# Performance work log

Hardware: AMD Instinct MI355X
Metric: run time of the kernel (lower is better)

## Reference

```python
import jax, jax.numpy as jnp
import numpy as np

EPS = 1e-7  # K.epsilon()
ROUTINGS = 3

def squash(v):
    # v: [..., dim_capsule]
    s2 = jnp.sum(jnp.square(v), axis=-1, keepdims=True)
    scale = s2 / (1.0 + s2) / jnp.sqrt(s2 + EPS)
    return scale * v

def setup_inputs() -> dict:
    key = jax.random.key(0)
    k1, k2 = jax.random.split(key)
    B, IN_CAPS, IN_DIM = 256, 1152, 8
    NUM_CAPS, DIM_CAPS = 10, 16
    inputs = jax.random.normal(k1, (B, IN_CAPS, IN_DIM), dtype=jnp.float32)
    W = jax.random.normal(k2, (NUM_CAPS, IN_CAPS, DIM_CAPS, IN_DIM), dtype=jnp.float32) * 0.05
    return {"inputs": inputs, "W": W}

def reference(inputs, W):
    # inputs: [B, I, Q]; W: [J, I, P, Q]
    # inputs_hat[b,j,i,p] = sum_q W[j,i,p,q] * inputs[b,i,q]
    inputs_hat = jnp.einsum('jipq,biq->bjip', W, inputs)  # [B, J, I, P]
    B, J, I, P = inputs_hat.shape
    b = jnp.zeros((B, J, I), dtype=inputs_hat.dtype)
    outputs = None
    for r in range(ROUTINGS):
        c = jax.nn.softmax(b, axis=1)                      # over num_capsule J
        s = jnp.einsum('bji,bjip->bjp', c, inputs_hat)     # [B, J, P]
        outputs = squash(s)
        if r < ROUTINGS - 1:
            b = b + jnp.einsum('bjp,bjip->bji', outputs, inputs_hat)
    return outputs
```

## Files before the change

kernel.cpp:

```cpp
#include <hip/hip_runtime.h>

typedef _Float16 h2 __attribute__((ext_vector_type(2)));
typedef _Float16 h8 __attribute__((ext_vector_type(8)));
typedef float f4 __attribute__((ext_vector_type(4)));

#define BB 256
#define II 1152
#define QQ 8
#define JJ 10
#define PP 16

#define BT 16
#define IT 8
#define NBT (BB / BT)
#define NIT (II / IT)
#define XRH 72
#define WTILE (IT * PP * QQ)

#define NW (JJ * II * PP * QQ)
#define NX (BB * II * QQ)
#define NS (BB * JJ * PP)
#define LOG2E 1.4426950408889634f

template <int CTRL>
__device__ __forceinline__ float dpp_add(float v) {
    int s = __builtin_bit_cast(int, v);
    int t = __builtin_amdgcn_update_dpp(0, s, CTRL, 0xF, 0xF, true);
    return v + __builtin_bit_cast(float, t);
}
__device__ __forceinline__ float row_sum16(float v) {
    v = dpp_add<0xB1>(v);
    v = dpp_add<0x4E>(v);
    v = dpp_add<0x124>(v);
    v = dpp_add<0x128>(v);
    return v;
}

__device__ __forceinline__ float dot8(h8 w, h8 x) {
    h2 w0 = __builtin_shufflevector(w, w, 0, 1), w1 = __builtin_shufflevector(w, w, 2, 3);
    h2 w2 = __builtin_shufflevector(w, w, 4, 5), w3 = __builtin_shufflevector(w, w, 6, 7);
    h2 x0 = __builtin_shufflevector(x, x, 0, 1), x1 = __builtin_shufflevector(x, x, 2, 3);
    h2 x2 = __builtin_shufflevector(x, x, 4, 5), x3 = __builtin_shufflevector(x, x, 6, 7);
    float acc = __builtin_amdgcn_fdot2(w0, x0, 0.0f, false);
    acc = __builtin_amdgcn_fdot2(w1, x1, acc, false);
    acc = __builtin_amdgcn_fdot2(w2, x2, acc, false);
    acc = __builtin_amdgcn_fdot2(w3, x3, acc, false);
    return acc;
}

__global__ __launch_bounds__(256) void prep_kernel(
    const float* __restrict__ X, const float* __restrict__ W,
    _Float16* __restrict__ Xh, _Float16* __restrict__ Wh,
    float* __restrict__ S)
{
    const int g = blockIdx.x * 256 + threadIdx.x;
    const int stride = gridDim.x * 256;
    typedef _Float16 h4 __attribute__((ext_vector_type(4)));
    for (int k = g; k < NW / 4; k += stride) {
        const float4 f = ((const float4*)W)[k];
        h4 o = { (_Float16)f.x, (_Float16)f.y, (_Float16)f.z, (_Float16)f.w };
        ((h4*)Wh)[k] = o;
    }
    for (int k = g; k < NX / 4; k += stride) {
        const float4 f = ((const float4*)X)[k];
        h4 o = { (_Float16)f.x, (_Float16)f.y, (_Float16)f.z, (_Float16)f.w };
        ((h4*)Xh)[k] = o;
    }
    const float4 z = {0.f, 0.f, 0.f, 0.f};
    for (int k = g; k < 3 * NS / 4; k += stride) ((float4*)S)[k] = z;
}

__global__ __launch_bounds__(256) void s0_mfma_kernel(
    const _Float16* __restrict__ Xh, const _Float16* __restrict__ Wh,
    float* __restrict__ S0)
{
    const int wid  = blockIdx.x * 4 + (threadIdx.x >> 6);
    const int lane = threadIdx.x & 63;
    const int bt  = wid / 80;
    const int rem = wid % 80;
    const int j   = rem >> 3;
    const int kc  = rem & 7;
    const int b0  = bt * 16;
    const int m    = lane & 15;
    const int quad = lane >> 4;
    const int ib   = kc * 144;

    const _Float16* ax = Xh + ((size_t)(b0 + m) * II + ib + quad) * QQ;
    const _Float16* bw = Wh + (((size_t)j * II + ib + quad) * PP + m) * QQ;

    f4 acc = {0.f, 0.f, 0.f, 0.f};
    for (int t = 0; t < 36; ++t) {
        const h8 a = *(const h8*)ax;
        const h8 b = *(const h8*)bw;
        acc = __builtin_amdgcn_mfma_f32_16x16x32_f16(a, b, acc, 0, 0, 0);
        ax += 4 * QQ;
        bw += (size_t)4 * PP * QQ;
    }
#pragma unroll
    for (int r = 0; r < 4; ++r) {
        const int row = quad * 4 + r;
        atomicAdd(&S0[((size_t)(b0 + row) * JJ + j) * PP + m], 0.1f * acc[r]);
    }
}

template <int R>
__global__ __launch_bounds__(256, 4) void pass_kernel(
    const _Float16* __restrict__ Xh,
    const _Float16* __restrict__ Wh,
    const float* __restrict__ Sprev,
    float* __restrict__ V0,
    float* __restrict__ Sout)
{
    __shared__ _Float16 ws[JJ * WTILE];
    __shared__ _Float16 xs[BT * XRH];

    const int bt = blockIdx.x & (NBT - 1);
    const int it = blockIdx.x >> 4;
    const int b0 = bt * BT;
    const int i0 = it * IT;
    const int tid = threadIdx.x;

    {
        const size_t jstride = (size_t)II * PP * QQ;
        const _Float16* wsrc = Wh + (size_t)i0 * PP * QQ;
#pragma unroll
        for (int k = 0; k < 5; ++k) {
            const int c = tid + k * 256;
            const int j = c >> 7;
            const int r = c & 127;
            *(h8*)(ws + j * WTILE + r * 8) = *(const h8*)(wsrc + j * jstride + r * 8);
        }
        if (tid < 128) {
            const int xb = tid >> 3;
            const int xr = tid & 7;
            *(h8*)(xs + xb * XRH + xr * 8) =
                *(const h8*)(Xh + ((size_t)(b0 + xb) * II + i0) * QQ + xr * 8);
        }
    }
    __syncthreads();

    const int b_l = tid >> 4;
    const int p   = tid & 15;
    const int b   = b0 + b_l;

    float vv[JJ];
#pragma unroll
    for (int j = 0; j < JJ; ++j) {
        const float sp = Sprev[((size_t)b * JJ + j) * PP + p];
        const float n2 = row_sum16(sp * sp);
        const float scale = n2 * __builtin_amdgcn_rcpf(1.0f + n2)
                               * __builtin_amdgcn_rsqf(n2 + 1e-7f);
        float v = sp * scale;
        if (R == 1) {
            if (it == 0) V0[((size_t)b * JJ + j) * PP + p] = v;
        } else {
            v += V0[((size_t)b * JJ + j) * PP + p];
        }
        vv[j] = v * LOG2E;
    }

    float sacc[JJ];
#pragma unroll
    for (int j = 0; j < JJ; ++j) sacc[j] = 0.0f;

    const _Float16* wb = ws + p * QQ;
    const _Float16* xb = xs + b_l * XRH;

#pragma unroll
    for (int i = 0; i < IT; ++i) {
        const h8 x8 = *(const h8*)(xb + i * QQ);

        float h[JJ];
#pragma unroll
        for (int j = 0; j < JJ; ++j)
            h[j] = dot8(*(const h8*)(wb + j * WTILE + i * PP * QQ), x8);

        float e[JJ];
#pragma unroll
        for (int j = 0; j < JJ; ++j) {
            const float bj = row_sum16(vv[j] * h[j]);
            e[j] = __builtin_amdgcn_exp2f(bj);
        }
        float s01 = e[0] + e[1], s23 = e[2] + e[3], s45 = e[4] + e[5],
              s67 = e[6] + e[7], s89 = e[8] + e[9];
        float t0 = s01 + s23, t1 = s45 + s67;
        const float sum = (t0 + t1) + s89;
        const float inv = __builtin_amdgcn_rcpf(sum);
#pragma unroll
        for (int j = 0; j < JJ; ++j) sacc[j] += (e[j] * inv) * h[j];
    }

#pragma unroll
    for (int j = 0; j < JJ; ++j)
        atomicAdd(&Sout[((size_t)b * JJ + j) * PP + p], sacc[j]);
}

__global__ __launch_bounds__(256) void squash_out_kernel(const float* __restrict__ S,
                                                         float* __restrict__ V)
{
    const int idx = blockIdx.x * blockDim.x + threadIdx.x;
    if (idx >= BB * JJ) return;
    const float4* sp = (const float4*)(S + idx * PP);
    float4 a = sp[0], b4 = sp[1], c4 = sp[2], d4 = sp[3];
    float s2 = a.x * a.x + a.y * a.y + a.z * a.z + a.w * a.w +
               b4.x * b4.x + b4.y * b4.y + b4.z * b4.z + b4.w * b4.w +
               c4.x * c4.x + c4.y * c4.y + c4.z * c4.z + c4.w * c4.w +
               d4.x * d4.x + d4.y * d4.y + d4.z * d4.z + d4.w * d4.w;
    const float scale = s2 / (1.0f + s2) / sqrtf(s2 + 1e-7f);
    a.x *= scale; a.y *= scale; a.z *= scale; a.w *= scale;
    b4.x *= scale; b4.y *= scale; b4.z *= scale; b4.w *= scale;
    c4.x *= scale; c4.y *= scale; c4.z *= scale; c4.w *= scale;
    d4.x *= scale; d4.y *= scale; d4.z *= scale; d4.w *= scale;
    float4* vp = (float4*)(V + idx * PP);
    vp[0] = a; vp[1] = b4; vp[2] = c4; vp[3] = d4;
}

extern "C" void kernel_launch(void* const* d_in, const int* in_sizes, int n_in,
                              void* d_out, int out_size, void* d_ws, size_t ws_size,
                              hipStream_t stream)
{
    const float* X = (const float*)d_in[0];
    const float* W = (const float*)d_in[1];
    float* out = (float*)d_out;

    _Float16* Xh = (_Float16*)d_ws;
    _Float16* Wh = Xh + NX;
    float* S0 = (float*)(Wh + NW);
    float* S1 = S0 + NS;
    float* S2 = S1 + NS;
    float* v0 = S2 + NS;

    const int grid = NBT * NIT;

    prep_kernel<<<1024, 256, 0, stream>>>(X, W, Xh, Wh, S0);
    s0_mfma_kernel<<<320, 256, 0, stream>>>(Xh, Wh, S0);
    pass_kernel<1><<<grid, 256, 0, stream>>>(Xh, Wh, S0, v0, S1);
    pass_kernel<2><<<grid, 256, 0, stream>>>(Xh, Wh, S1, v0, S2);
    squash_out_kernel<<<10, 256, 0, stream>>>(S2, out);
}
```

Measured before the change: 134.2 us.

## Move routing pass dot products onto MFMA using transposed fp16 weight copy

Rewrites the routing pass kernel so both the agreement logits (v·W·x) and the weighted sum into S use 16x16x32 f16 MFMA instructions instead of per-thread fdot2 loops with DPP row reductions. To feed the first MFMA, the prep kernel now also writes a transposed fp16 copy of W (p innermost). The block no longer stages W in shared memory but reads W directly from global, and it keeps x transposed in fp32 in LDS. The transpose uses uncoalesced scalar reads of W in prep. The pass also issues more atomics and rounds the routing coefficients and v to fp16, which may cost precision.

```diff
diff --git a/kernel.cpp b/kernel.cpp
--- a/kernel.cpp
+++ b/kernel.cpp
@@ -15,11 +15,14 @@
 #define NBT (BB / BT)
 #define NIT (II / IT)
 #define XRH 72
-#define WTILE (IT * PP * QQ)
+#define VHR 168
+#define XTQ 17
+#define XTI 136
 
 #define NW (JJ * II * PP * QQ)
 #define NX (BB * II * QQ)
 #define NS (BB * JJ * PP)
+#define JSTRIDE ((size_t)II * PP * QQ)
 #define LOG2E 1.4426950408889634f
 
 template <int CTRL>
@@ -35,23 +38,15 @@
     v = dpp_add<0x128>(v);
     return v;
 }
-
-__device__ __forceinline__ float dot8(h8 w, h8 x) {
-    h2 w0 = __builtin_shufflevector(w, w, 0, 1), w1 = __builtin_shufflevector(w, w, 2, 3);
-    h2 w2 = __builtin_shufflevector(w, w, 4, 5), w3 = __builtin_shufflevector(w, w, 6, 7);
-    h2 x0 = __builtin_shufflevector(x, x, 0, 1), x1 = __builtin_shufflevector(x, x, 2, 3);
-    h2 x2 = __builtin_shufflevector(x, x, 4, 5), x3 = __builtin_shufflevector(x, x, 6, 7);
-    float acc = __builtin_amdgcn_fdot2(w0, x0, 0.0f, false);
-    acc = __builtin_amdgcn_fdot2(w1, x1, acc, false);
-    acc = __builtin_amdgcn_fdot2(w2, x2, acc, false);
-    acc = __builtin_amdgcn_fdot2(w3, x3, acc, false);
-    return acc;
+__device__ __forceinline__ float swz_xor16(float v) {
+    int s = __builtin_bit_cast(int, v);
+    return __builtin_bit_cast(float, __builtin_amdgcn_ds_swizzle(s, 0x401F));
 }
 
 __global__ __launch_bounds__(256) void prep_kernel(
     const float* __restrict__ X, const float* __restrict__ W,
     _Float16* __restrict__ Xh, _Float16* __restrict__ Wh,
-    float* __restrict__ S)
+    _Float16* __restrict__ Wt, float* __restrict__ S)
 {
     const int g = blockIdx.x * 256 + threadIdx.x;
     const int stride = gridDim.x * 256;
@@ -60,6 +55,10 @@
         const float4 f = ((const float4*)W)[k];
         h4 o = { (_Float16)f.x, (_Float16)f.y, (_Float16)f.z, (_Float16)f.w };
         ((h4*)Wh)[k] = o;
+    }
+    for (int k = g; k < NW; k += stride) {
+        const int p = k & 15, q = (k >> 4) & 7, ji = k >> 7;
+        Wt[k] = (_Float16)W[((size_t)ji * 16 + p) * 8 + q];
     }
     for (int k = g; k < NX / 4; k += stride) {
         const float4 f = ((const float4*)X)[k];
@@ -97,22 +96,22 @@
         bw += (size_t)4 * PP * QQ;
     }
 #pragma unroll
-    for (int r = 0; r < 4; ++r) {
-        const int row = quad * 4 + r;
-        atomicAdd(&S0[((size_t)(b0 + row) * JJ + j) * PP + m], 0.1f * acc[r]);
-    }
+    for (int r = 0; r < 4; ++r)
+        atomicAdd(&S0[((size_t)(b0 + quad * 4 + r) * JJ + j) * PP + m], 0.1f * acc[r]);
 }
 
 template <int R>
 __global__ __launch_bounds__(256, 4) void pass_kernel(
     const _Float16* __restrict__ Xh,
     const _Float16* __restrict__ Wh,
+    const _Float16* __restrict__ Wt,
     const float* __restrict__ Sprev,
     float* __restrict__ V0,
     float* __restrict__ Sout)
 {
-    __shared__ _Float16 ws[JJ * WTILE];
     __shared__ _Float16 xs[BT * XRH];
+    __shared__ float    xT[IT * XTI];
+    __shared__ _Float16 vh[BT * VHR];
 
     const int bt = blockIdx.x & (NBT - 1);
     const int it = blockIdx.x >> 4;
@@ -120,79 +119,92 @@
     const int i0 = it * IT;
     const int tid = threadIdx.x;
 
+    if (tid < 128) {
+        const int xb = tid >> 3, xr = tid & 7;
+        *(h8*)(xs + xb * XRH + xr * 8) =
+            *(const h8*)(Xh + ((size_t)(b0 + xb) * II + i0) * QQ + xr * 8);
+    }
+#pragma unroll
+    for (int r = 0; r < 4; ++r) {
+        const int idx = tid + r * 256;
+        const int b = idx & 15, q = (idx >> 4) & 7, il = idx >> 7;
+        xT[il * XTI + q * XTQ + b] =
+            (float)Xh[((size_t)(b0 + b) * II + i0 + il) * QQ + q];
+    }
     {
-        const size_t jstride = (size_t)II * PP * QQ;
-        const _Float16* wsrc = Wh + (size_t)i0 * PP * QQ;
-#pragma unroll
-        for (int k = 0; k < 5; ++k) {
-            const int c = tid + k * 256;
-            const int j = c >> 7;
-            const int r = c & 127;
-            *(h8*)(ws + j * WTILE + r * 8) = *(const h8*)(wsrc + j * jstride + r * 8);
+        const int b_l = tid >> 4, p = tid & 15;
+        const int b = b0 + b_l;
+#pragma unroll
+        for (int j = 0; j < JJ; ++j) {
+            const float sp = Sprev[((size_t)b * JJ + j) * PP + p];
+            const float n2 = row_sum16(sp * sp);
+            const float sc = n2 * __builtin_amdgcn_rcpf(1.0f + n2)
+                                * __builtin_amdgcn_rsqf(n2 + 1e-7f);
+            float v = sp * sc;
+            if (R == 1) {
+                if (it == 0) V0[((size_t)b * JJ + j) * PP + p] = v;
+            } else {
+                v += V0[((size_t)b * JJ + j) * PP + p];
+            }
+            vh[b_l * VHR + j * 16 + p] = (_Float16)(v * LOG2E);
         }
-        if (tid < 128) {
-            const int xb = tid >> 3;
-            const int xr = tid & 7;
-            *(h8*)(xs + xb * XRH + xr * 8) =
-                *(const h8*)(Xh + ((size_t)(b0 + xb) * II + i0) * QQ + xr * 8);
-        }
     }
     __syncthreads();
 
-    const int b_l = tid >> 4;
-    const int p   = tid & 15;
-    const int b   = b0 + b_l;
-
-    float vv[JJ];
+    const int lane = tid & 63;
+    const int wv   = tid >> 6;
+    const int quad = lane >> 4;
+    const int l15  = lane & 15;
+    const h8 hz = {(_Float16)0, (_Float16)0, (_Float16)0, (_Float16)0,
+                   (_Float16)0, (_Float16)0, (_Float16)0, (_Float16)0};
+
+    const int il = 2 * wv + (quad >> 1);
+    float xv0, xv1, xv2, xv3;
+    {
+        const float* xp = xT + il * XTI + ((quad & 1) * 4) * XTQ + l15;
+        xv0 = xp[0]; xv1 = xp[XTQ]; xv2 = xp[2 * XTQ]; xv3 = xp[3 * XTQ];
+    }
+    const int iA = i0 + 2 * wv + (l15 >> 3);
+    const _Float16* abase = Wt + ((size_t)iA * QQ + (l15 & 7)) * PP + (quad & 1) * 8;
+    const _Float16* vbase = vh + l15 * VHR + (quad & 1) * 8;
+
+    float lg[JJ];
 #pragma unroll
     for (int j = 0; j < JJ; ++j) {
-        const float sp = Sprev[((size_t)b * JJ + j) * PP + p];
-        const float n2 = row_sum16(sp * sp);
-        const float scale = n2 * __builtin_amdgcn_rcpf(1.0f + n2)
-                               * __builtin_amdgcn_rsqf(n2 + 1e-7f);
-        float v = sp * scale;
-        if (R == 1) {
-            if (it == 0) V0[((size_t)b * JJ + j) * PP + p] = v;
-        } else {
-            v += V0[((size_t)b * JJ + j) * PP + p];
-        }
-        vv[j] = v * LOG2E;
-    }
-
-    float sacc[JJ];
-#pragma unroll
-    for (int j = 0; j < JJ; ++j) sacc[j] = 0.0f;
-
-    const _Float16* wb = ws + p * QQ;
-    const _Float16* xb = xs + b_l * XRH;
-
-#pragma unroll
-    for (int i = 0; i < IT; ++i) {
-        const h8 x8 = *(const h8*)(xb + i * QQ);
-
-        float h[JJ];
-#pragma unroll
-        for (int j = 0; j < JJ; ++j)
-            h[j] = dot8(*(const h8*)(wb + j * WTILE + i * PP * QQ), x8);
-
-        float e[JJ];
-#pragma unroll
-        for (int j = 0; j < JJ; ++j) {
-            const float bj = row_sum16(vv[j] * h[j]);
-            e[j] = __builtin_amdgcn_exp2f(bj);
-        }
-        float s01 = e[0] + e[1], s23 = e[2] + e[3], s45 = e[4] + e[5],
-              s67 = e[6] + e[7], s89 = e[8] + e[9];
-        float t0 = s01 + s23, t1 = s45 + s67;
-        const float sum = (t0 + t1) + s89;
-        const float inv = __builtin_amdgcn_rcpf(sum);
-#pragma unroll
-        for (int j = 0; j < JJ; ++j) sacc[j] += (e[j] * inv) * h[j];
-    }
-
-#pragma unroll
-    for (int j = 0; j < JJ; ++j)
-        atomicAdd(&Sout[((size_t)b * JJ + j) * PP + p], sacc[j]);
+        const h8 a  = *(const h8*)(abase + (size_t)j * JSTRIDE);
+        h8 bv = *(const h8*)(vbase + j * 16);
+        if (quad >= 2) bv = hz;
+        f4 acc = {0.f, 0.f, 0.f, 0.f};
+        acc = __builtin_amdgcn_mfma_f32_16x16x32_f16(a, bv, acc, 0, 0, 0);
+        const float part = acc[0] * xv0 + acc[1] * xv1 + acc[2] * xv2 + acc[3] * xv3;
+        lg[j] = part + swz_xor16(part);
+    }
+
+    float e[JJ];
+#pragma unroll
+    for (int j = 0; j < JJ; ++j) e[j] = __builtin_amdgcn_exp2f(lg[j]);
+    float s01 = e[0] + e[1], s23 = e[2] + e[3], s45 = e[4] + e[5],
+          s67 = e[6] + e[7], s89 = e[8] + e[9];
+    const float sum = ((s01 + s23) + (s45 + s67)) + s89;
+    const float inv = __builtin_amdgcn_rcpf(sum);
+
+    const int ig = i0 + 2 * wv + (quad >> 1);
+    const h8 x8 = *(const h8*)(xs + l15 * XRH + (2 * wv + (quad >> 1)) * 8);
+    const _Float16* bbase = Wh + ((size_t)ig * PP + l15) * QQ;
+
+#pragma unroll
+    for (int j = 0; j < JJ; ++j) {
+        const _Float16 ch = (_Float16)(e[j] * inv);
+        const h8 cs8 = {ch, ch, ch, ch, ch, ch, ch, ch};
+        const h8 a2 = x8 * cs8;
+        h8 b2 = *(const h8*)(bbase + (size_t)j * JSTRIDE);
+        if (quad & 1) b2 = hz;
+        f4 acc = {0.f, 0.f, 0.f, 0.f};
+        acc = __builtin_amdgcn_mfma_f32_16x16x32_f16(a2, b2, acc, 0, 0, 0);
+#pragma unroll
+        for (int r = 0; r < 4; ++r)
+            atomicAdd(&Sout[((size_t)(b0 + quad * 4 + r) * JJ + j) * PP + l15], acc[r]);
+    }
 }
 
 __global__ __launch_bounds__(256) void squash_out_kernel(const float* __restrict__ S,
@@ -225,16 +237,17 @@
 
     _Float16* Xh = (_Float16*)d_ws;
     _Float16* Wh = Xh + NX;
-    float* S0 = (float*)(Wh + NW);
+    _Float16* Wt = Wh + NW;
+    float* S0 = (float*)(Wt + NW);
     float* S1 = S0 + NS;
     float* S2 = S1 + NS;
     float* v0 = S2 + NS;
 
     const int grid = NBT * NIT;
 
-    prep_kernel<<<1024, 256, 0, stream>>>(X, W, Xh, Wh, S0);
+    prep_kernel<<<1024, 256, 0, stream>>>(X, W, Xh, Wh, Wt, S0);
     s0_mfma_kernel<<<320, 256, 0, stream>>>(Xh, Wh, S0);
-    pass_kernel<1><<<grid, 256, 0, stream>>>(Xh, Wh, S0, v0, S1);
-    pass_kernel<2><<<grid, 256, 0, stream>>>(Xh, Wh, S1, v0, S2);
+    pass_kernel<1><<<grid, 256, 0, stream>>>(Xh, Wh, Wt, S0, v0, S1);
+    pass_kernel<2><<<grid, 256, 0, stream>>>(Xh, Wh, Wt, S1, v0, S2);
     squash_out_kernel<<<10, 256, 0, stream>>>(S2, out);
 }
```

Result: slower. 267.3 us (+99.2%).

## Process two batch rows per thread in routing passes to reuse W tile

Applied to the files above, without the earlier changes.

Doubles the batch tile per block from 16 to 32 so each thread handles two batch elements, reusing every LDS-loaded W vector for two dot products. The block count per pass halves, which cuts the redundant loads of the W tile into shared memory and the number of blocks issuing atomics. In exchange each thread holds twice the registers (two sets of v, h, e and accumulators), which may reduce occupancy under the launch bound of 4 blocks.

```diff
diff --git a/kernel.cpp b/kernel.cpp
--- a/kernel.cpp
+++ b/kernel.cpp
@@ -10,7 +10,7 @@
 #define JJ 10
 #define PP 16
 
-#define BT 16
+#define BT 32
 #define IT 8
 #define NBT (BB / BT)
 #define NIT (II / IT)
@@ -97,10 +97,8 @@
         bw += (size_t)4 * PP * QQ;
     }
 #pragma unroll
-    for (int r = 0; r < 4; ++r) {
-        const int row = quad * 4 + r;
-        atomicAdd(&S0[((size_t)(b0 + row) * JJ + j) * PP + m], 0.1f * acc[r]);
-    }
+    for (int r = 0; r < 4; ++r)
+        atomicAdd(&S0[((size_t)(b0 + quad * 4 + r) * JJ + j) * PP + m], 0.1f * acc[r]);
 }
 
 template <int R>
@@ -115,7 +113,7 @@
     __shared__ _Float16 xs[BT * XRH];
 
     const int bt = blockIdx.x & (NBT - 1);
-    const int it = blockIdx.x >> 4;
+    const int it = blockIdx.x >> 3;
     const int b0 = bt * BT;
     const int i0 = it * IT;
     const int tid = threadIdx.x;
@@ -130,69 +128,93 @@
             const int r = c & 127;
             *(h8*)(ws + j * WTILE + r * 8) = *(const h8*)(wsrc + j * jstride + r * 8);
         }
-        if (tid < 128) {
-            const int xb = tid >> 3;
-            const int xr = tid & 7;
-            *(h8*)(xs + xb * XRH + xr * 8) =
-                *(const h8*)(Xh + ((size_t)(b0 + xb) * II + i0) * QQ + xr * 8);
-        }
+        const int xb = tid >> 3;
+        const int xr = tid & 7;
+        *(h8*)(xs + xb * XRH + xr * 8) =
+            *(const h8*)(Xh + ((size_t)(b0 + xb) * II + i0) * QQ + xr * 8);
     }
     __syncthreads();
 
     const int b_l = tid >> 4;
     const int p   = tid & 15;
-    const int b   = b0 + b_l;
-
-    float vv[JJ];
+    const int bA  = b0 + b_l;
+    const int bB  = bA + 16;
+
+    float vvA[JJ], vvB[JJ];
 #pragma unroll
     for (int j = 0; j < JJ; ++j) {
-        const float sp = Sprev[((size_t)b * JJ + j) * PP + p];
-        const float n2 = row_sum16(sp * sp);
-        const float scale = n2 * __builtin_amdgcn_rcpf(1.0f + n2)
-                               * __builtin_amdgcn_rsqf(n2 + 1e-7f);
-        float v = sp * scale;
+        const float spA = Sprev[((size_t)bA * JJ + j) * PP + p];
+        const float spB = Sprev[((size_t)bB * JJ + j) * PP + p];
+        const float nA = row_sum16(spA * spA);
+        const float nB = row_sum16(spB * spB);
+        const float scA = nA * __builtin_amdgcn_rcpf(1.0f + nA)
+                             * __builtin_amdgcn_rsqf(nA + 1e-7f);
+        const float scB = nB * __builtin_amdgcn_rcpf(1.0f + nB)
+                             * __builtin_amdgcn_rsqf(nB + 1e-7f);
+        float vA = spA * scA;
+        float vB = spB * scB;
         if (R == 1) {
-            if (it == 0) V0[((size_t)b * JJ + j) * PP + p] = v;
+            if (it == 0) {
+                V0[((size_t)bA * JJ + j) * PP + p] = vA;
+                V0[((size_t)bB * JJ + j) * PP + p] = vB;
+            }
         } else {
-            v += V0[((size_t)b * JJ + j) * PP + p];
-        }
-        vv[j] = v * LOG2E;
-    }
-
-    float sacc[JJ];
-#pragma unroll
-    for (int j = 0; j < JJ; ++j) sacc[j] = 0.0f;
+            vA += V0[((size_t)bA * JJ + j) * PP + p];
+            vB += V0[((size_t)bB * JJ + j) * PP + p];
+        }
+        vvA[j] = vA * LOG2E;
+        vvB[j] = vB * LOG2E;
+    }
+
+    float saccA[JJ], saccB[JJ];
+#pragma unroll
+    for (int j = 0; j < JJ; ++j) { saccA[j] = 0.0f; saccB[j] = 0.0f; }
 
     const _Float16* wb = ws + p * QQ;
-    const _Float16* xb = xs + b_l * XRH;
+    const _Float16* xa = xs + b_l * XRH;
+    const _Float16* xbp = xs + (b_l + 16) * XRH;
 
 #pragma unroll
     for (int i = 0; i < IT; ++i) {
-        const h8 x8 = *(const h8*)(xb + i * QQ);
-
-        float h[JJ];
-#pragma unroll
-        for (int j = 0; j < JJ; ++j)
-            h[j] = dot8(*(const h8*)(wb + j * WTILE + i * PP * QQ), x8);
-
-        float e[JJ];
+        const h8 x8A = *(const h8*)(xa + i * QQ);
+        const h8 x8B = *(const h8*)(xbp + i * QQ);
+
+        float hA[JJ], hB[JJ];
 #pragma unroll
         for (int j = 0; j < JJ; ++j) {
-            const float bj = row_sum16(vv[j] * h[j]);
-            e[j] = __builtin_amdgcn_exp2f(bj);
-        }
-        float s01 = e[0] + e[1], s23 = e[2] + e[3], s45 = e[4] + e[5],
-              s67 = e[6] + e[7], s89 = e[8] + e[9];
-        float t0 = s01 + s23, t1 = s45 + s67;
-        const float sum = (t0 + t1) + s89;
-        const float inv = __builtin_amdgcn_rcpf(sum);
-#pragma unroll
-        for (int j = 0; j < JJ; ++j) sacc[j] += (e[j] * inv) * h[j];
-    }
-
-#pragma unroll
-    for (int j = 0; j < JJ; ++j)
-        atomicAdd(&Sout[((size_t)b * JJ + j) * PP + p], sacc[j]);
+            const h8 w8 = *(const h8*)(wb + j * WTILE + i * PP * QQ);
+            hA[j] = dot8(w8, x8A);
+            hB[j] = dot8(w8, x8B);
+        }
+
+        float eA[JJ], eB[JJ];
+#pragma unroll
+        for (int j = 0; j < JJ; ++j) {
+            const float bjA = row_sum16(vvA[j] * hA[j]);
+            const float bjB = row_sum16(vvB[j] * hB[j]);
+            eA[j] = __builtin_amdgcn_exp2f(bjA);
+            eB[j] = __builtin_amdgcn_exp2f(bjB);
+        }
+        float aA0 = (eA[0] + eA[1]) + (eA[2] + eA[3]);
+        float aA1 = (eA[4] + eA[5]) + (eA[6] + eA[7]);
+        const float sumA = (aA0 + aA1) + (eA[8] + eA[9]);
+        float aB0 = (eB[0] + eB[1]) + (eB[2] + eB[3]);
+        float aB1 = (eB[4] + eB[5]) + (eB[6] + eB[7]);
+        const float sumB = (aB0 + aB1) + (eB[8] + eB[9]);
+        const float invA = __builtin_amdgcn_rcpf(sumA);
+        const float invB = __builtin_amdgcn_rcpf(sumB);
+#pragma unroll
+        for (int j = 0; j < JJ; ++j) {
+            saccA[j] += (eA[j] * invA) * hA[j];
+            saccB[j] += (eB[j] * invB) * hB[j];
+        }
+    }
+
+#pragma unroll
+    for (int j = 0; j < JJ; ++j) {
+        atomicAdd(&Sout[((size_t)bA * JJ + j) * PP + p], saccA[j]);
+        atomicAdd(&Sout[((size_t)bB * JJ + j) * PP + p], saccB[j]);
+    }
 }
 
 __global__ __launch_bounds__(256) void squash_out_kernel(const float* __restrict__ S,
```

Result: slower. 154.7 us (+15.2%).

## Precompute squashed routing vectors in separate kernel and pack logit reductions into fp16

Applied to the files above, without the earlier changes.

Moves the per-block squash of the previous S (with its DPP row reductions and rcp/rsq) out of pass_kernel into a small vv_kernel run once per routing pass, so each of the many pass blocks only loads ready-made scaled vectors. The per-i logit row reductions now run on two j values packed as fp16 pairs, which halves the DPP adds. This adds two kernel launches and extra global traffic, and the fp16 logit sums lose precision before exp2.

```diff
diff --git a/kernel.cpp b/kernel.cpp
--- a/kernel.cpp
+++ b/kernel.cpp
@@ -33,6 +33,19 @@
     v = dpp_add<0x4E>(v);
     v = dpp_add<0x124>(v);
     v = dpp_add<0x128>(v);
+    return v;
+}
+template <int CTRL>
+__device__ __forceinline__ h2 dpp_add_pk(h2 v) {
+    int s = __builtin_bit_cast(int, v);
+    int t = __builtin_amdgcn_update_dpp(0, s, CTRL, 0xF, 0xF, true);
+    return v + __builtin_bit_cast(h2, t);
+}
+__device__ __forceinline__ h2 row_sum16_pk(h2 v) {
+    v = dpp_add_pk<0xB1>(v);
+    v = dpp_add_pk<0x4E>(v);
+    v = dpp_add_pk<0x124>(v);
+    v = dpp_add_pk<0x128>(v);
     return v;
 }
 
@@ -97,18 +110,33 @@
         bw += (size_t)4 * PP * QQ;
     }
 #pragma unroll
-    for (int r = 0; r < 4; ++r) {
-        const int row = quad * 4 + r;
-        atomicAdd(&S0[((size_t)(b0 + row) * JJ + j) * PP + m], 0.1f * acc[r]);
-    }
-}
-
-template <int R>
+    for (int r = 0; r < 4; ++r)
+        atomicAdd(&S0[((size_t)(b0 + quad * 4 + r) * JJ + j) * PP + m], 0.1f * acc[r]);
+}
+
+template <int MODE>
+__global__ __launch_bounds__(256) void vv_kernel(
+    const float* __restrict__ S, float* __restrict__ V0raw,
+    float* __restrict__ VV)
+{
+    const int idx = blockIdx.x * 256 + threadIdx.x;
+    const float s = S[idx];
+    const float n2 = row_sum16(s * s);
+    const float sc = n2 * __builtin_amdgcn_rcpf(1.0f + n2)
+                        * __builtin_amdgcn_rsqf(n2 + 1e-7f);
+    const float v = s * sc;
+    if (MODE == 0) {
+        V0raw[idx] = v;
+        VV[idx] = v * LOG2E;
+    } else {
+        VV[idx] = (v + V0raw[idx]) * LOG2E;
+    }
+}
+
 __global__ __launch_bounds__(256, 4) void pass_kernel(
     const _Float16* __restrict__ Xh,
     const _Float16* __restrict__ Wh,
-    const float* __restrict__ Sprev,
-    float* __restrict__ V0,
+    const float* __restrict__ VV,
     float* __restrict__ Sout)
 {
     __shared__ _Float16 ws[JJ * WTILE];
@@ -145,19 +173,8 @@
 
     float vv[JJ];
 #pragma unroll
-    for (int j = 0; j < JJ; ++j) {
-        const float sp = Sprev[((size_t)b * JJ + j) * PP + p];
-        const float n2 = row_sum16(sp * sp);
-        const float scale = n2 * __builtin_amdgcn_rcpf(1.0f + n2)
-                               * __builtin_amdgcn_rsqf(n2 + 1e-7f);
-        float v = sp * scale;
-        if (R == 1) {
-            if (it == 0) V0[((size_t)b * JJ + j) * PP + p] = v;
-        } else {
-            v += V0[((size_t)b * JJ + j) * PP + p];
-        }
-        vv[j] = v * LOG2E;
-    }
+    for (int j = 0; j < JJ; ++j)
+        vv[j] = VV[((size_t)b * JJ + j) * PP + p];
 
     float sacc[JJ];
 #pragma unroll
@@ -177,14 +194,17 @@
 
         float e[JJ];
 #pragma unroll
-        for (int j = 0; j < JJ; ++j) {
-            const float bj = row_sum16(vv[j] * h[j]);
-            e[j] = __builtin_amdgcn_exp2f(bj);
+        for (int jp = 0; jp < JJ; jp += 2) {
+            const h2 pk = __builtin_bit_cast(h2,
+                __builtin_amdgcn_cvt_pkrtz(vv[jp] * h[jp],
+                                           vv[jp + 1] * h[jp + 1]));
+            const h2 r = row_sum16_pk(pk);
+            e[jp]     = __builtin_amdgcn_exp2f((float)r.x);
+            e[jp + 1] = __builtin_amdgcn_exp2f((float)r.y);
         }
-        float s01 = e[0] + e[1], s23 = e[2] + e[3], s45 = e[4] + e[5],
-              s67 = e[6] + e[7], s89 = e[8] + e[9];
-        float t0 = s01 + s23, t1 = s45 + s67;
-        const float sum = (t0 + t1) + s89;
+        float a0 = (e[0] + e[1]) + (e[2] + e[3]);
+        float a1 = (e[4] + e[5]) + (e[6] + e[7]);
+        const float sum = (a0 + a1) + (e[8] + e[9]);
         const float inv = __builtin_amdgcn_rcpf(sum);
 #pragma unroll
         for (int j = 0; j < JJ; ++j) sacc[j] += (e[j] * inv) * h[j];
@@ -228,13 +248,18 @@
     float* S0 = (float*)(Wh + NW);
     float* S1 = S0 + NS;
     float* S2 = S1 + NS;
-    float* v0 = S2 + NS;
-
-    const int grid = NBT * NIT;
+    float* V0raw = S2 + NS;
+    float* VV1   = V0raw + NS;
+    float* VV2   = VV1 + NS;
+
+    const int grid  = NBT * NIT;
+    const int vgrid = NS / 256;
 
     prep_kernel<<<1024, 256, 0, stream>>>(X, W, Xh, Wh, S0);
     s0_mfma_kernel<<<320, 256, 0, stream>>>(Xh, Wh, S0);
-    pass_kernel<1><<<grid, 256, 0, stream>>>(Xh, Wh, S0, v0, S1);
-    pass_kernel<2><<<grid, 256, 0, stream>>>(Xh, Wh, S1, v0, S2);
+    vv_kernel<0><<<vgrid, 256, 0, stream>>>(S0, V0raw, VV1);
+    pass_kernel<<<grid, 256, 0, stream>>>(Xh, Wh, VV1, S1);
+    vv_kernel<1><<<vgrid, 256, 0, stream>>>(S1, V0raw, VV2);
+    pass_kernel<<<grid, 256, 0, stream>>>(Xh, Wh, VV2, S2);
     squash_out_kernel<<<10, 256, 0, stream>>>(S2, out);
 }
```

Result: no change. 133.3 us (-0.6%).
